# Kernel optimization log

Hardware: AMD Instinct MI355X
Metric: run time of the kernel (lower is better)

The kernel has to match this reference:

```python
import jax, jax.numpy as jnp
import numpy as np

SIZE = 32000
PAD_IDX = 0
SMOOTHING = 0.1
CONFIDENCE = 1.0 - SMOOTHING
NUM_EXPERTS = 8
LOAD_COEF = 0.01
Z_COEF = 0.001
NORMALIZE_LENGTH = True


def setup_inputs() -> dict:
    key = jax.random.key(0)
    k0, k1, k2, k3, k4 = jax.random.split(key, 5)
    B, S, K = 2, 2048, 2
    return {
        "x": jax.random.normal(k0, (B, S, SIZE), dtype=jnp.float32),
        "topk_values": jax.random.uniform(k1, (B, S, K), dtype=jnp.float32),
        "gate_logits": jax.random.normal(k2, (B, S, NUM_EXPERTS), dtype=jnp.float32),
        "target": jax.random.randint(k3, (B, S), 0, SIZE, dtype=jnp.int64),
        "topk_indices": jax.random.randint(k4, (B, S, K), 0, NUM_EXPERTS, dtype=jnp.int64),
    }


def reference(x, topk_values, gate_logits, target, topk_indices):
    # ---- label smoothing KLDiv ----
    xf = x.reshape(-1, SIZE)            # [N, V]
    t = target.reshape(-1)              # [N]
    N = xf.shape[0]
    ignore = t == PAD_IDX               # [N]
    total = N - ignore.sum()
    t0 = jnp.where(ignore, 0, t)
    smooth_val = SMOOTHING / (SIZE - 1)
    # true_dist built under torch.no_grad -> constant
    true_dist = jnp.full((N, SIZE), smooth_val, dtype=xf.dtype)
    true_dist = true_dist.at[jnp.arange(N), t0].set(CONFIDENCE)
    true_dist = jax.lax.stop_gradient(true_dist)
    logp = jax.nn.log_softmax(xf, axis=1)
    # KLDivLoss(reduction='none'): target * (log(target) - input)
    kl = true_dist * (jnp.log(true_dist) - logp)
    kl = jnp.where(ignore[:, None], jnp.zeros((), xf.dtype), kl)
    denom = total.astype(xf.dtype) if NORMALIZE_LENGTH else jnp.asarray(x.shape[0], xf.dtype)
    label_smoothing_loss = kl.sum() / denom

    # ---- load balancing loss (fused histogram instead of per-expert loop) ----
    # torch version uses .item() per expert -> fully detached from autodiff
    flat_idx = topk_indices.reshape(-1)
    expert_loads = jnp.zeros(NUM_EXPERTS, xf.dtype).at[flat_idx].add(1.0)
    logits_sum = jnp.zeros(NUM_EXPERTS, xf.dtype).at[flat_idx].add(topk_values.reshape(-1))
    num_elements = topk_indices.shape[0] * topk_indices.shape[1]
    load_loss = jax.lax.stop_gradient(
        (NUM_EXPERTS / num_elements) * (expert_loads * logits_sum).sum()
    )

    # ---- router z-loss ----
    router_z_loss = jnp.mean(jnp.square(jax.nn.logsumexp(gate_logits, axis=-1)))

    return label_smoothing_loss + LOAD_COEF * load_loss + Z_COEF * router_z_loss
```

## Files before the change

### kernel.cpp

```cpp
#include <hip/hip_runtime.h>
#include <hip/hip_bf16.h>
#include <math.h>

#define SIZE_V 32000
#define NROWS  4096
#define NEXP   8
#define NTOPK  8192
#define RBLK   512


__device__ inline float waveReduceSum(float v) {
#pragma unroll
    for (int off = 32; off; off >>= 1) v += __shfl_xor(v, off, 64);
    return v;
}

__global__ __launch_bounds__(RBLK) void row_kernel(const float* __restrict__ x,
                                                   const int* __restrict__ target,
                                                   const float* __restrict__ gate,
                                                   float* __restrict__ klrow,
                                                   float* __restrict__ zrow,
                                                   float self_ent, float smooth) {
    __shared__ float smS[8];
    __shared__ float smX[8];

    const int row = blockIdx.x;
    const int tid = threadIdx.x;
    const float4* xr = (const float4*)(x + (size_t)row * SIZE_V);

    int t = 0;
    float xt = 0.f;
    float4 ga = {0, 0, 0, 0}, gb = {0, 0, 0, 0};
    if (tid == 0) {
        t  = target[row];
        xt = x[(size_t)row * SIZE_V + t];
        const float4* gr = (const float4*)(gate + (size_t)row * NEXP);
        ga = gr[0];
        gb = gr[1];
    }

    float sAcc[5] = {0, 0, 0, 0, 0};
    float xAcc[5] = {0, 0, 0, 0, 0};
    float4 cur0, cur1, cur2, cur3, cur4;
    float4 nxt0, nxt1, nxt2, nxt3, nxt4;
    float4 vt = {0, 0, 0, 0};
    const bool hasTail = (tid < 320);

    cur0 = xr[tid + 0 * RBLK];
    cur1 = xr[tid + 1 * RBLK];
    cur2 = xr[tid + 2 * RBLK];
    cur3 = xr[tid + 3 * RBLK];
    cur4 = xr[tid + 4 * RBLK];

    for (int j = 0; j < 3; ++j) {
        if (j < 2) {
            const int base = (j + 1) * 5;
            nxt0 = xr[tid + (base + 0) * RBLK];
            nxt1 = xr[tid + (base + 1) * RBLK];
            nxt2 = xr[tid + (base + 2) * RBLK];
            nxt3 = xr[tid + (base + 3) * RBLK];
            nxt4 = xr[tid + (base + 4) * RBLK];
        } else if (hasTail) {
            vt = xr[tid + 15 * RBLK];
        }
        sAcc[0] += (__expf(cur0.x) + __expf(cur0.y)) + (__expf(cur0.z) + __expf(cur0.w));
        xAcc[0] += (cur0.x + cur0.y) + (cur0.z + cur0.w);
        sAcc[1] += (__expf(cur1.x) + __expf(cur1.y)) + (__expf(cur1.z) + __expf(cur1.w));
        xAcc[1] += (cur1.x + cur1.y) + (cur1.z + cur1.w);
        sAcc[2] += (__expf(cur2.x) + __expf(cur2.y)) + (__expf(cur2.z) + __expf(cur2.w));
        xAcc[2] += (cur2.x + cur2.y) + (cur2.z + cur2.w);
        sAcc[3] += (__expf(cur3.x) + __expf(cur3.y)) + (__expf(cur3.z) + __expf(cur3.w));
        xAcc[3] += (cur3.x + cur3.y) + (cur3.z + cur3.w);
        sAcc[4] += (__expf(cur4.x) + __expf(cur4.y)) + (__expf(cur4.z) + __expf(cur4.w));
        xAcc[4] += (cur4.x + cur4.y) + (cur4.z + cur4.w);
        cur0 = nxt0; cur1 = nxt1; cur2 = nxt2; cur3 = nxt3; cur4 = nxt4;
    }
    if (hasTail) {
        sAcc[0] += (__expf(vt.x) + __expf(vt.y)) + (__expf(vt.z) + __expf(vt.w));
        xAcc[0] += (vt.x + vt.y) + (vt.z + vt.w);
    }
    float s  = ((sAcc[0] + sAcc[1]) + (sAcc[2] + sAcc[3])) + sAcc[4];
    float sx = ((xAcc[0] + xAcc[1]) + (xAcc[2] + xAcc[3])) + xAcc[4];

    const int lane = tid & 63, wid = tid >> 6;
    s  = waveReduceSum(s);
    sx = waveReduceSum(sx);
    if (lane == 0) { smS[wid] = s; smX[wid] = sx; }
    __syncthreads();

    if (tid == 0) {
        float S  = ((smS[0] + smS[1]) + (smS[2] + smS[3]))
                 + ((smS[4] + smS[5]) + (smS[6] + smS[7]));
        float SX = ((smX[0] + smX[1]) + (smX[2] + smX[3]))
                 + ((smX[4] + smX[5]) + (smX[6] + smX[7]));
        float logZ = __logf(S);
        float kl = 0.f;
        if (t != 0) {
            float sum_logp = SX - (float)SIZE_V * logZ;
            float logp_t = xt - logZ;
            kl = self_ent - (smooth * (sum_logp - logp_t) + 0.9f * logp_t);
        }
        klrow[row] = kl;

        float mx = fmaxf(fmaxf(fmaxf(ga.x, ga.y), fmaxf(ga.z, ga.w)),
                         fmaxf(fmaxf(gb.x, gb.y), fmaxf(gb.z, gb.w)));
        float se = __expf(ga.x - mx) + __expf(ga.y - mx) + __expf(ga.z - mx) + __expf(ga.w - mx)
                 + __expf(gb.x - mx) + __expf(gb.y - mx) + __expf(gb.z - mx) + __expf(gb.w - mx);
        float lse = mx + __logf(se);
        zrow[row] = lse * lse;
    }
}

__global__ __launch_bounds__(1024) void tail_kernel(const float* __restrict__ klrow,
                                                    const float* __restrict__ zrow,
                                                    const int* __restrict__ target,
                                                    const int* __restrict__ tidx,
                                                    const float* __restrict__ tval,
                                                    float* __restrict__ out) {
    __shared__ float sm[16][20];
    const int tid = threadIdx.x;

    float4 kv = ((const float4*)klrow)[tid];
    float4 zv = ((const float4*)zrow)[tid];
    int4   tv = ((const int4*)target)[tid];
    float kacc = (kv.x + kv.y) + (kv.z + kv.w);
    float zacc = (zv.x + zv.y) + (zv.z + zv.w);
    float cacc = ((tv.x != 0) ? 1.f : 0.f) + ((tv.y != 0) ? 1.f : 0.f)
               + ((tv.z != 0) ? 1.f : 0.f) + ((tv.w != 0) ? 1.f : 0.f);

    const int4*   ti4 = (const int4*)tidx;
    const float4* tv4 = (const float4*)tval;
    int4   e0 = ti4[tid * 2], e1 = ti4[tid * 2 + 1];
    float4 v0 = tv4[tid * 2], v1 = tv4[tid * 2 + 1];
    int   ee[8] = {e0.x, e0.y, e0.z, e0.w, e1.x, e1.y, e1.z, e1.w};
    float vv[8] = {v0.x, v0.y, v0.z, v0.w, v1.x, v1.y, v1.z, v1.w};

    float cnt[NEXP]  = {0, 0, 0, 0, 0, 0, 0, 0};
    float vsum[NEXP] = {0, 0, 0, 0, 0, 0, 0, 0};
#pragma unroll
    for (int i = 0; i < 8; i++) {
#pragma unroll
        for (int k = 0; k < NEXP; k++) {
            bool hit = (ee[i] == k);
            cnt[k]  += hit ? 1.f : 0.f;
            vsum[k] += hit ? vv[i] : 0.f;
        }
    }

    kacc = waveReduceSum(kacc);
    cacc = waveReduceSum(cacc);
    zacc = waveReduceSum(zacc);
#pragma unroll
    for (int k = 0; k < NEXP; k++) {
        cnt[k]  = waveReduceSum(cnt[k]);
        vsum[k] = waveReduceSum(vsum[k]);
    }

    const int lane = tid & 63, wid = tid >> 6;
    if (lane == 0) {
        sm[wid][0] = kacc;
        sm[wid][1] = cacc;
        sm[wid][2] = zacc;
#pragma unroll
        for (int k = 0; k < NEXP; k++) {
            sm[wid][3 + k]  = cnt[k];
            sm[wid][11 + k] = vsum[k];
        }
    }
    __syncthreads();

    if (tid == 0) {
        float KL = 0.f, TOT = 0.f, Z = 0.f;
        float C[NEXP] = {0, 0, 0, 0, 0, 0, 0, 0};
        float V[NEXP] = {0, 0, 0, 0, 0, 0, 0, 0};
        for (int w = 0; w < 16; w++) {
            KL += sm[w][0];
            TOT += sm[w][1];
            Z  += sm[w][2];
#pragma unroll
            for (int k = 0; k < NEXP; k++) {
                C[k] += sm[w][3 + k];
                V[k] += sm[w][11 + k];
            }
        }
        float dot = 0.f;
#pragma unroll
        for (int k = 0; k < NEXP; k++) dot += C[k] * V[k];

        float label = KL / TOT;
        float load  = ((float)NEXP / (float)NROWS) * dot;
        float z     = Z / (float)NROWS;
        out[0] = label + 0.01f * load + 0.001f * z;
    }
}

extern "C" void kernel_launch(void* const* d_in, const int* in_sizes, int n_in,
                              void* d_out, int out_size, void* d_ws, size_t ws_size,
                              hipStream_t stream) {
    const float* x      = (const float*)d_in[0];
    const float* tval   = (const float*)d_in[1];
    const float* gate   = (const float*)d_in[2];
    const int*   target = (const int*)d_in[3];
    const int*   tidx   = (const int*)d_in[4];
    float* out = (float*)d_out;
    float* klrow = (float*)d_ws;
    float* zrow  = (float*)d_ws + NROWS;

    const double sv = 0.1 / (double)(SIZE_V - 1);
    const float self_ent = (float)((double)(SIZE_V - 1) * sv * log(sv) + 0.9 * log(0.9));

    hipLaunchKernelGGL(row_kernel, dim3(NROWS), dim3(RBLK), 0, stream,
                       x, target, gate, klrow, zrow, self_ent, (float)sv);
    hipLaunchKernelGGL(tail_kernel, dim3(1), dim3(1024), 0, stream,
                       klrow, zrow, target, tidx, tval, out);
}
```

Baseline: 100.1 us.

## Process multiple rows per block with cross-row prefetch of next row

```diff
diff --git a/kernel.cpp b/kernel.cpp
--- a/kernel.cpp
+++ b/kernel.cpp
@@ -7,6 +7,7 @@
 #define NEXP   8
 #define NTOPK  8192
 #define RBLK   512
+#define RPB    8
 
 
 __device__ inline float waveReduceSum(float v) {
@@ -15,99 +16,111 @@
     return v;
 }
 
-__global__ __launch_bounds__(RBLK) void row_kernel(const float* __restrict__ x,
-                                                   const int* __restrict__ target,
-                                                   const float* __restrict__ gate,
-                                                   float* __restrict__ klrow,
-                                                   float* __restrict__ zrow,
-                                                   float self_ent, float smooth) {
-    __shared__ float smS[8];
-    __shared__ float smX[8];
-
-    const int row = blockIdx.x;
-    const int tid = threadIdx.x;
+__global__ __launch_bounds__(RBLK, 4) void row_kernel(const float* __restrict__ x,
+                                                      const int* __restrict__ target,
+                                                      const float* __restrict__ gate,
+                                                      float* __restrict__ klrow,
+                                                      float* __restrict__ zrow,
+                                                      float self_ent, float smooth) {
+    __shared__ float smS[2][8];
+    __shared__ float smX[2][8];
+
+    const int tid  = threadIdx.x;
+    const int lane = tid & 63, wid = tid >> 6;
+    const bool hasTail = (tid < 320);
+
+    int row = blockIdx.x * RPB;
     const float4* xr = (const float4*)(x + (size_t)row * SIZE_V);
 
-    int t = 0;
-    float xt = 0.f;
-    float4 ga = {0, 0, 0, 0}, gb = {0, 0, 0, 0};
-    if (tid == 0) {
-        t  = target[row];
-        xt = x[(size_t)row * SIZE_V + t];
-        const float4* gr = (const float4*)(gate + (size_t)row * NEXP);
-        ga = gr[0];
-        gb = gr[1];
-    }
-
-    float sAcc[5] = {0, 0, 0, 0, 0};
-    float xAcc[5] = {0, 0, 0, 0, 0};
-    float4 cur0, cur1, cur2, cur3, cur4;
-    float4 nxt0, nxt1, nxt2, nxt3, nxt4;
-    float4 vt = {0, 0, 0, 0};
-    const bool hasTail = (tid < 320);
-
-    cur0 = xr[tid + 0 * RBLK];
-    cur1 = xr[tid + 1 * RBLK];
-    cur2 = xr[tid + 2 * RBLK];
-    cur3 = xr[tid + 3 * RBLK];
-    cur4 = xr[tid + 4 * RBLK];
-
-    for (int j = 0; j < 3; ++j) {
-        if (j < 2) {
-            const int base = (j + 1) * 5;
-            nxt0 = xr[tid + (base + 0) * RBLK];
-            nxt1 = xr[tid + (base + 1) * RBLK];
-            nxt2 = xr[tid + (base + 2) * RBLK];
-            nxt3 = xr[tid + (base + 3) * RBLK];
-            nxt4 = xr[tid + (base + 4) * RBLK];
-        } else if (hasTail) {
-            vt = xr[tid + 15 * RBLK];
-        }
-        sAcc[0] += (__expf(cur0.x) + __expf(cur0.y)) + (__expf(cur0.z) + __expf(cur0.w));
-        xAcc[0] += (cur0.x + cur0.y) + (cur0.z + cur0.w);
-        sAcc[1] += (__expf(cur1.x) + __expf(cur1.y)) + (__expf(cur1.z) + __expf(cur1.w));
-        xAcc[1] += (cur1.x + cur1.y) + (cur1.z + cur1.w);
-        sAcc[2] += (__expf(cur2.x) + __expf(cur2.y)) + (__expf(cur2.z) + __expf(cur2.w));
-        xAcc[2] += (cur2.x + cur2.y) + (cur2.z + cur2.w);
-        sAcc[3] += (__expf(cur3.x) + __expf(cur3.y)) + (__expf(cur3.z) + __expf(cur3.w));
-        xAcc[3] += (cur3.x + cur3.y) + (cur3.z + cur3.w);
-        sAcc[4] += (__expf(cur4.x) + __expf(cur4.y)) + (__expf(cur4.z) + __expf(cur4.w));
-        xAcc[4] += (cur4.x + cur4.y) + (cur4.z + cur4.w);
-        cur0 = nxt0; cur1 = nxt1; cur2 = nxt2; cur3 = nxt3; cur4 = nxt4;
-    }
-    if (hasTail) {
-        sAcc[0] += (__expf(vt.x) + __expf(vt.y)) + (__expf(vt.z) + __expf(vt.w));
-        xAcc[0] += (vt.x + vt.y) + (vt.z + vt.w);
-    }
-    float s  = ((sAcc[0] + sAcc[1]) + (sAcc[2] + sAcc[3])) + sAcc[4];
-    float sx = ((xAcc[0] + xAcc[1]) + (xAcc[2] + xAcc[3])) + xAcc[4];
-
-    const int lane = tid & 63, wid = tid >> 6;
-    s  = waveReduceSum(s);
-    sx = waveReduceSum(sx);
-    if (lane == 0) { smS[wid] = s; smX[wid] = sx; }
-    __syncthreads();
-
-    if (tid == 0) {
-        float S  = ((smS[0] + smS[1]) + (smS[2] + smS[3]))
-                 + ((smS[4] + smS[5]) + (smS[6] + smS[7]));
-        float SX = ((smX[0] + smX[1]) + (smX[2] + smX[3]))
-                 + ((smX[4] + smX[5]) + (smX[6] + smX[7]));
-        float logZ = __logf(S);
-        float kl = 0.f;
-        if (t != 0) {
-            float sum_logp = SX - (float)SIZE_V * logZ;
-            float logp_t = xt - logZ;
-            kl = self_ent - (smooth * (sum_logp - logp_t) + 0.9f * logp_t);
-        }
-        klrow[row] = kl;
-
-        float mx = fmaxf(fmaxf(fmaxf(ga.x, ga.y), fmaxf(ga.z, ga.w)),
-                         fmaxf(fmaxf(gb.x, gb.y), fmaxf(gb.z, gb.w)));
-        float se = __expf(ga.x - mx) + __expf(ga.y - mx) + __expf(ga.z - mx) + __expf(ga.w - mx)
-                 + __expf(gb.x - mx) + __expf(gb.y - mx) + __expf(gb.z - mx) + __expf(gb.w - mx);
-        float lse = mx + __logf(se);
-        zrow[row] = lse * lse;
+    float4 cur0 = xr[tid + 0 * RBLK];
+    float4 cur1 = xr[tid + 1 * RBLK];
+    float4 cur2 = xr[tid + 2 * RBLK];
+    float4 cur3 = xr[tid + 3 * RBLK];
+    float4 cur4 = xr[tid + 4 * RBLK];
+    float4 nxt0 = {0,0,0,0}, nxt1 = {0,0,0,0}, nxt2 = {0,0,0,0},
+           nxt3 = {0,0,0,0}, nxt4 = {0,0,0,0};
+
+    for (int r = 0; r < RPB; ++r, ++row) {
+        int t = 0;
+        float xt = 0.f;
+        float4 ga = {0,0,0,0}, gb = {0,0,0,0};
+        if (tid == 0) {
+            t  = target[row];
+            xt = x[(size_t)row * SIZE_V + t];
+            const float4* gr = (const float4*)(gate + (size_t)row * NEXP);
+            ga = gr[0];
+            gb = gr[1];
+        }
+
+        float sAcc[5] = {0, 0, 0, 0, 0};
+        float xAcc[5] = {0, 0, 0, 0, 0};
+        float4 vt = {0, 0, 0, 0};
+
+        for (int j = 0; j < 3; ++j) {
+            if (j < 2) {
+                const int base = (j + 1) * 5;
+                nxt0 = xr[tid + (base + 0) * RBLK];
+                nxt1 = xr[tid + (base + 1) * RBLK];
+                nxt2 = xr[tid + (base + 2) * RBLK];
+                nxt3 = xr[tid + (base + 3) * RBLK];
+                nxt4 = xr[tid + (base + 4) * RBLK];
+            } else {
+                if (hasTail) vt = xr[tid + 15 * RBLK];
+                if (r < RPB - 1) {
+                    const float4* xr2 = xr + (SIZE_V / 4);
+                    nxt0 = xr2[tid + 0 * RBLK];
+                    nxt1 = xr2[tid + 1 * RBLK];
+                    nxt2 = xr2[tid + 2 * RBLK];
+                    nxt3 = xr2[tid + 3 * RBLK];
+                    nxt4 = xr2[tid + 4 * RBLK];
+                }
+            }
+            sAcc[0] += (__expf(cur0.x) + __expf(cur0.y)) + (__expf(cur0.z) + __expf(cur0.w));
+            xAcc[0] += (cur0.x + cur0.y) + (cur0.z + cur0.w);
+            sAcc[1] += (__expf(cur1.x) + __expf(cur1.y)) + (__expf(cur1.z) + __expf(cur1.w));
+            xAcc[1] += (cur1.x + cur1.y) + (cur1.z + cur1.w);
+            sAcc[2] += (__expf(cur2.x) + __expf(cur2.y)) + (__expf(cur2.z) + __expf(cur2.w));
+            xAcc[2] += (cur2.x + cur2.y) + (cur2.z + cur2.w);
+            sAcc[3] += (__expf(cur3.x) + __expf(cur3.y)) + (__expf(cur3.z) + __expf(cur3.w));
+            xAcc[3] += (cur3.x + cur3.y) + (cur3.z + cur3.w);
+            sAcc[4] += (__expf(cur4.x) + __expf(cur4.y)) + (__expf(cur4.z) + __expf(cur4.w));
+            xAcc[4] += (cur4.x + cur4.y) + (cur4.z + cur4.w);
+            cur0 = nxt0; cur1 = nxt1; cur2 = nxt2; cur3 = nxt3; cur4 = nxt4;
+        }
+        if (hasTail) {
+            sAcc[0] += (__expf(vt.x) + __expf(vt.y)) + (__expf(vt.z) + __expf(vt.w));
+            xAcc[0] += (vt.x + vt.y) + (vt.z + vt.w);
+        }
+        float s  = ((sAcc[0] + sAcc[1]) + (sAcc[2] + sAcc[3])) + sAcc[4];
+        float sx = ((xAcc[0] + xAcc[1]) + (xAcc[2] + xAcc[3])) + xAcc[4];
+
+        s  = waveReduceSum(s);
+        sx = waveReduceSum(sx);
+        if (lane == 0) { smS[r & 1][wid] = s; smX[r & 1][wid] = sx; }
+        __syncthreads();
+
+        if (tid == 0) {
+            float S  = ((smS[r & 1][0] + smS[r & 1][1]) + (smS[r & 1][2] + smS[r & 1][3]))
+                     + ((smS[r & 1][4] + smS[r & 1][5]) + (smS[r & 1][6] + smS[r & 1][7]));
+            float SX = ((smX[r & 1][0] + smX[r & 1][1]) + (smX[r & 1][2] + smX[r & 1][3]))
+                     + ((smX[r & 1][4] + smX[r & 1][5]) + (smX[r & 1][6] + smX[r & 1][7]));
+            float logZ = __logf(S);
+            float kl = 0.f;
+            if (t != 0) {
+                float sum_logp = SX - (float)SIZE_V * logZ;
+                float logp_t = xt - logZ;
+                kl = self_ent - (smooth * (sum_logp - logp_t) + 0.9f * logp_t);
+            }
+            klrow[row] = kl;
+
+            float mx = fmaxf(fmaxf(fmaxf(ga.x, ga.y), fmaxf(ga.z, ga.w)),
+                             fmaxf(fmaxf(gb.x, gb.y), fmaxf(gb.z, gb.w)));
+            float se = __expf(ga.x - mx) + __expf(ga.y - mx) + __expf(ga.z - mx) + __expf(ga.w - mx)
+                     + __expf(gb.x - mx) + __expf(gb.y - mx) + __expf(gb.z - mx) + __expf(gb.w - mx);
+            float lse = mx + __logf(se);
+            zrow[row] = lse * lse;
+        }
+        xr += (SIZE_V / 4);
     }
 }
 
@@ -209,7 +222,7 @@
     const double sv = 0.1 / (double)(SIZE_V - 1);
     const float self_ent = (float)((double)(SIZE_V - 1) * sv * log(sv) + 0.9 * log(0.9));
 
-    hipLaunchKernelGGL(row_kernel, dim3(NROWS), dim3(RBLK), 0, stream,
+    hipLaunchKernelGGL(row_kernel, dim3(NROWS / RPB), dim3(RBLK), 0, stream,
                        x, target, gate, klrow, zrow, self_ent, (float)sv);
     hipLaunchKernelGGL(tail_kernel, dim3(1), dim3(1024), 0, stream,
                        klrow, zrow, target, tidx, tval, out);
```

Measured after the change: 107.6 us. 1.07x slower.
